# Kernel tuning notes

Measured on AMD Instinct MI355X. Metric: run time of the kernel, lower is better.

## Reference

```python
import jax, jax.numpy as jnp
import numpy as np

WD, WH, WW = 1, 7, 7
N = WD * WH * WW  # 49 tokens per window
LN_EPS = 1e-5


def _make_rel_coords_table():
    rd = np.arange(-(WD - 1), WD, dtype=np.float32)
    rh = np.arange(-(WH - 1), WH, dtype=np.float32)
    rw = np.arange(-(WW - 1), WW, dtype=np.float32)
    g = np.stack(np.meshgrid(rd, rh, rw, indexing='ij'), axis=-1)  # (2wd-1,2wh-1,2ww-1,3)
    eps = 1e-6
    g = g / (np.array([WD, WH, WW], np.float32) - (1.0 - eps))
    g = g * 8.0
    g = np.sign(g) * np.log2(np.abs(g) + 1.0) / np.log2(8.0)
    return g[None].astype(np.float32)  # (1,2wd-1,2wh-1,2ww-1,3)


def _make_rel_pos_index():
    coords = np.stack(np.meshgrid(np.arange(WD), np.arange(WH), np.arange(WW), indexing='ij'))
    cf = coords.reshape(3, -1)  # (3,N)
    rel = cf[:, :, None] - cf[:, None, :]  # (3,N,N)
    rel = rel.transpose(1, 2, 0).astype(np.int64)
    rel[..., 0] += WD - 1
    rel[..., 1] += WH - 1
    rel[..., 2] += WW - 1
    rel[..., 0] *= (2 * WH - 1) * (2 * WW - 1)
    rel[..., 1] *= 2 * WW - 1
    return rel.sum(-1).astype(np.int32)  # (N,N)


def setup_inputs() -> dict:
    key = jax.random.key(0)
    ks = jax.random.split(key, 8)
    B, D, H, W, C = 4, 8, 56, 56, 256
    nh, hid = 8, 4 * C

    def init_w(k, shape, fan_in):
        return (jax.random.normal(k, shape, jnp.float32) / np.sqrt(fan_in)).astype(jnp.float32)

    inp = {
        'x': jax.random.normal(ks[0], (B, D, H, W, C), jnp.float32),
        'qkv_w': init_w(ks[1], (3 * C, C), C),
        'q_bias': jnp.zeros((C,), jnp.float32),
        'v_bias': jnp.zeros((C,), jnp.float32),
        'logit_scale': jnp.full((nh, 1, 1), np.log(10.0), jnp.float32),
        'cpb_w1': init_w(ks[2], (512, 3), 3),
        'cpb_b1': jnp.zeros((512,), jnp.float32),
        'cpb_w2': init_w(ks[3], (nh, 512), 512),
        'proj_w': init_w(ks[4], (C, C), C),
        'proj_b': jnp.zeros((C,), jnp.float32),
        'norm1_g': jnp.ones((C,), jnp.float32),
        'norm1_b': jnp.zeros((C,), jnp.float32),
        'fc1_w': init_w(ks[5], (hid, C), C),
        'fc1_b': jnp.zeros((hid,), jnp.float32),
        'fc2_w': init_w(ks[6], (C, hid), hid),
        'fc2_b': jnp.zeros((C,), jnp.float32),
        'norm2_g': jnp.ones((C,), jnp.float32),
        'norm2_b': jnp.zeros((C,), jnp.float32),
        'rel_coords_table': jnp.asarray(_make_rel_coords_table()),
        'rel_pos_index': jnp.asarray(_make_rel_pos_index()),
    }
    return inp


def _layernorm(x, g, b):
    mu = jnp.mean(x, axis=-1, keepdims=True)
    var = jnp.mean(jnp.square(x - mu), axis=-1, keepdims=True)
    return (x - mu) * jax.lax.rsqrt(var + LN_EPS) * g + b


def _l2norm(x):
    # F.normalize(dim=-1): x / max(||x||, 1e-12)
    n = jnp.sqrt(jnp.sum(jnp.square(x), axis=-1, keepdims=True))
    return x / jnp.maximum(n, 1e-12)


def _forward(x, qkv_w, q_bias, v_bias, logit_scale, cpb_w1, cpb_b1, cpb_w2,
             proj_w, proj_b, norm1_g, norm1_b, fc1_w, fc1_b, fc2_w, fc2_b,
             norm2_g, norm2_b, rel_coords_table, rel_pos_index):
    B, D, H, W, C = x.shape
    nh = logit_scale.shape[0]
    hd = C // nh

    # ---- window partition: (B,D,H,W,C) -> (B_, N, C)
    xw = x.reshape(B, D // WD, WD, H // WH, WH, W // WW, WW, C)
    xw = xw.transpose(0, 1, 3, 5, 2, 4, 6, 7).reshape(-1, N, C)
    Bw = xw.shape[0]

    # ---- qkv with (q_bias, 0, v_bias)
    qkv_bias = jnp.concatenate([q_bias, jnp.zeros_like(q_bias), v_bias])
    qkv = xw @ qkv_w.T + qkv_bias  # (Bw,N,3C)
    qkv = qkv.reshape(Bw, N, 3, nh, hd).transpose(2, 0, 3, 1, 4)
    q, k, v = qkv[0], qkv[1], qkv[2]  # (Bw,nh,N,hd)

    # ---- cosine attention with clamped learned logit scale
    attn = jnp.einsum('bhnd,bhmd->bhnm', _l2norm(q), _l2norm(k))
    scale = jnp.exp(jnp.minimum(logit_scale, jnp.float32(np.log(100.0))))  # (nh,1,1)
    attn = attn * scale

    # ---- CPB-MLP relative position bias
    t = rel_coords_table.reshape(-1, 3)
    hcpb = jax.nn.relu(t @ cpb_w1.T + cpb_b1)
    table = hcpb @ cpb_w2.T  # (T, nh)
    rpb = table[rel_pos_index.reshape(-1)].reshape(N, N, nh).transpose(2, 0, 1)
    rpb = 16.0 * jax.nn.sigmoid(rpb)
    attn = attn + rpb[None]

    attn = jax.nn.softmax(attn, axis=-1)
    out = jnp.einsum('bhnm,bhmd->bhnd', attn, v)
    out = out.transpose(0, 2, 1, 3).reshape(Bw, N, C)
    out = out @ proj_w.T + proj_b

    # ---- window reverse
    xr = out.reshape(B, D // WD, H // WH, W // WW, WD, WH, WW, C)
    xr = xr.transpose(0, 1, 4, 2, 5, 3, 6, 7).reshape(B, D, H, W, C)

    # ---- Swin-v2 post-norm residuals
    x = x + _layernorm(xr, norm1_g, norm1_b)
    h = jax.nn.gelu(x @ fc1_w.T + fc1_b, approximate=False)
    y = h @ fc2_w.T + fc2_b
    x = x + _layernorm(y, norm2_g, norm2_b)
    return x


def reference(x, qkv_w, q_bias, v_bias, logit_scale, cpb_w1, cpb_b1, cpb_w2,
              proj_w, proj_b, norm1_g, norm1_b, fc1_w, fc1_b, fc2_w, fc2_b,
              norm2_g, norm2_b, rel_coords_table, rel_pos_index):
    return _forward(x, qkv_w, q_bias, v_bias, logit_scale, cpb_w1, cpb_b1, cpb_w2,
                    proj_w, proj_b, norm1_g, norm1_b, fc1_w, fc1_b, fc2_w, fc2_b,
                    norm2_g, norm2_b, rel_coords_table, rel_pos_index)
```

## Files before the change

### kernel.cpp

```cpp
#include <hip/hip_runtime.h>
#include <hip/hip_bf16.h>

typedef __attribute__((ext_vector_type(8))) short short8_t;
typedef __attribute__((ext_vector_type(4))) float f32x4;

__device__ __forceinline__ float bf2f(unsigned short u) {
    return __uint_as_float(((unsigned)u) << 16);
}
__device__ __forceinline__ unsigned short f2bf(float f) {
    __hip_bfloat16 h = __float2bfloat16(f);
    return *reinterpret_cast<unsigned short*>(&h);
}

__device__ __forceinline__ float fast_gelu(float v) {
    float ax = fabsf(v) * 0.70710678118f;
    float t  = __builtin_amdgcn_rcpf(1.f + 0.3275911f * ax);
    float poly = t * (0.254829592f + t * (-0.284496736f + t * (1.421413741f
               + t * (-1.453152027f + t * 1.061405429f))));
    float e  = __expf(-ax * ax);
    float er = 1.f - poly * e;
    float s  = (v >= 0.f) ? er : -er;
    return 0.5f * v * (1.f + s);
}

__device__ __forceinline__ void async16(const unsigned short* g, unsigned short* l) {
    __builtin_amdgcn_global_load_lds(
        (const __attribute__((address_space(1))) unsigned int*)g,
        (__attribute__((address_space(3))) unsigned int*)l,
        16, 0, 0);
}

__device__ __forceinline__ int win_row_to_token(int r) {
    int wb = r / 49, n = r - wb * 49;
    int wq = wb & 7, hb = (wb >> 3) & 7, d = (wb >> 6) & 7, b = wb >> 9;
    int hh = n / 7, ww2 = n - hh * 7;
    return ((b * 8 + d) * 56 + hb * 7 + hh) * 56 + wq * 7 + ww2;
}

__global__ __launch_bounds__(256) void conv_kernel(
    const float* __restrict__ src, unsigned short* __restrict__ dst, int n4)
{
    int stride = gridDim.x * 256;
    for (int i = blockIdx.x * 256 + threadIdx.x; i < n4; i += stride) {
        float4 v = *reinterpret_cast<const float4*>(&src[(size_t)i * 4]);
        short4 o;
        o.x = (short)f2bf(v.x); o.y = (short)f2bf(v.y);
        o.z = (short)f2bf(v.z); o.w = (short)f2bf(v.w);
        *reinterpret_cast<short4*>(&dst[(size_t)i * 4]) = o;
    }
}

__global__ __launch_bounds__(256) void conv4_kernel(
    const float* __restrict__ s0, unsigned short* __restrict__ d0, int n0,
    const float* __restrict__ s1, unsigned short* __restrict__ d1, int n1,
    const float* __restrict__ s2, unsigned short* __restrict__ d2, int n2,
    const float* __restrict__ s3, unsigned short* __restrict__ d3, int n3)
{
    int stride = gridDim.x * 256;
    int total = n0 + n1 + n2 + n3;
    for (int i = blockIdx.x * 256 + threadIdx.x; i < total; i += stride) {
        const float* s; unsigned short* d; int j = i;
        if (j < n0) { s = s0; d = d0; }
        else if ((j -= n0) < n1) { s = s1; d = d1; }
        else if ((j -= n1) < n2) { s = s2; d = d2; }
        else { j -= n2; s = s3; d = d3; }
        float4 v = *reinterpret_cast<const float4*>(&s[(size_t)j * 4]);
        short4 o;
        o.x = (short)f2bf(v.x); o.y = (short)f2bf(v.y);
        o.z = (short)f2bf(v.z); o.w = (short)f2bf(v.w);
        *reinterpret_cast<short4*>(&d[(size_t)j * 4]) = o;
    }
}

__global__ __launch_bounds__(256) void prep_table_kernel(
    const float* __restrict__ w1, const float* __restrict__ b1,
    const float* __restrict__ w2, const float* __restrict__ tabin,
    float* __restrict__ tableg)
{
    const int i = blockIdx.x;
    const int t = threadIdx.x;
    const float c0 = tabin[i * 3], c1 = tabin[i * 3 + 1], c2 = tabin[i * 3 + 2];
    float part[8] = {0.f, 0.f, 0.f, 0.f, 0.f, 0.f, 0.f, 0.f};
    for (int j = t; j < 512; j += 256) {
        float hv = fmaxf(c0 * w1[j * 3] + c1 * w1[j * 3 + 1] + c2 * w1[j * 3 + 2] + b1[j], 0.f);
        #pragma unroll
        for (int h = 0; h < 8; ++h) part[h] += hv * w2[h * 512 + j];
    }
    #pragma unroll
    for (int h = 0; h < 8; ++h) {
        float v = part[h];
        v += __shfl_xor(v, 1);  v += __shfl_xor(v, 2);  v += __shfl_xor(v, 4);
        v += __shfl_xor(v, 8);  v += __shfl_xor(v, 16); v += __shfl_xor(v, 32);
        part[h] = v;
    }
    __shared__ float red[4][8];
    const int wv = t >> 6, lane = t & 63;
    if (lane == 0) {
        #pragma unroll
        for (int h = 0; h < 8; ++h) red[wv][h] = part[h];
    }
    __syncthreads();
    if (t < 8) tableg[i * 8 + t] = red[0][t] + red[1][t] + red[2][t] + red[3][t];
}

__global__ __launch_bounds__(256) void prep_expand_kernel(
    const float* __restrict__ logit_scale,
    const float* __restrict__ qb, const float* __restrict__ vb,
    const int* __restrict__ rpi, const float* __restrict__ tableg,
    float* __restrict__ scales, float* __restrict__ rpbf,
    float* __restrict__ qkvb)
{
    const int stride = gridDim.x * 256;
    const int gt = blockIdx.x * 256 + threadIdx.x;
    if (gt < 8) scales[gt] = expf(fminf(logit_scale[gt], 4.6051702f));
    for (int i = gt; i < 768; i += stride) {
        float o;
        if (i < 256) o = qb[i];
        else if (i < 512) o = 0.f;
        else o = vb[i - 512];
        qkvb[i] = o;
    }
    for (int e = gt; e < 32768; e += stride) {
        int h = e >> 12, rem = e & 4095;
        int mi = rem >> 10, ji = (rem >> 8) & 3;
        int r16 = (rem >> 4) & 15, g4 = (rem >> 2) & 3, r = rem & 3;
        int i = mi * 16 + g4 * 4 + r, j = ji * 16 + r16;
        float val = 0.f;
        if (i < 49 && j < 49) {
            float xv = tableg[rpi[i * 49 + j] * 8 + h];
            val = 16.f / (1.f + expf(-xv));
        }
        rpbf[e] = val;
    }
}

template<int ACT, int SCATTER>
__global__ __launch_bounds__(256) void gemm_kernel(
    const unsigned short* __restrict__ A, const unsigned short* __restrict__ W,
    const float* __restrict__ bias, unsigned short* __restrict__ C,
    int M, int N, int K, int ntn)
{
    __shared__ unsigned short smem[16384];
    const int tid = threadIdx.x;
    const int lane = tid & 63, wv = tid >> 6;
    const int wr = wv >> 1, wc = wv & 1;
    const int nwg = gridDim.x;
    const int virt = (blockIdx.x & 7) * (nwg >> 3) + (blockIdx.x >> 3);
    const int bn = virt % ntn, bm = virt / ntn;
    const size_t arow0 = (size_t)bm * 128;
    const size_t brow0 = (size_t)bn * 128;
    const int r16 = lane & 15, g4 = lane >> 4;
    const int srow_l = lane >> 2;
    const int sgran  = (lane & 3) ^ ((srow_l >> 1) & 3);
    f32x4 acc[4][4] = {};

    auto STAGE = [&](int buf, int kt) {
        unsigned short* As = smem + buf * 4096;
        unsigned short* Bs = smem + 8192 + buf * 4096;
        #pragma unroll
        for (int i = 0; i < 2; ++i) {
            int row0 = wv * 32 + i * 16;
            async16(&A[(arow0 + row0 + srow_l) * (size_t)K + kt + sgran * 8], &As[row0 * 32]);
            async16(&W[(brow0 + row0 + srow_l) * (size_t)K + kt + sgran * 8], &Bs[row0 * 32]);
        }
    };
    auto COMPUTE = [&](int buf) {
        unsigned short* As = smem + buf * 4096;
        unsigned short* Bs = smem + 8192 + buf * 4096;
        short8_t af[4], bfr[4];
        const int gsw = g4 ^ ((r16 >> 1) & 3);
        #pragma unroll
        for (int m = 0; m < 4; ++m) {
            int row = wr * 64 + m * 16 + r16;
            af[m] = *reinterpret_cast<const short8_t*>(&As[row * 32 + gsw * 8]);
        }
        #pragma unroll
        for (int n = 0; n < 4; ++n) {
            int row = wc * 64 + n * 16 + r16;
            bfr[n] = *reinterpret_cast<const short8_t*>(&Bs[row * 32 + gsw * 8]);
        }
        #pragma unroll
        for (int m = 0; m < 4; ++m)
            #pragma unroll
            for (int n = 0; n < 4; ++n)
                acc[m][n] = __builtin_amdgcn_mfma_f32_16x16x32_bf16(af[m], bfr[n], acc[m][n], 0, 0, 0);
    };

    const int nk = K >> 5;
    STAGE(0, 0);
    STAGE(1, 32);
    int cur = 0;
    for (int ks = 0; ks < nk - 1; ++ks) {
        asm volatile("s_waitcnt vmcnt(4)" ::: "memory");
        __builtin_amdgcn_sched_barrier(0);
        asm volatile("s_barrier" ::: "memory");
        COMPUTE(cur);
        __builtin_amdgcn_sched_barrier(0);
        asm volatile("s_barrier" ::: "memory");
        if (ks + 2 < nk) STAGE(cur, (ks + 2) << 5);
        cur ^= 1;
    }
    asm volatile("s_waitcnt vmcnt(0)" ::: "memory");
    __builtin_amdgcn_sched_barrier(0);
    asm volatile("s_barrier" ::: "memory");
    COMPUTE(cur);
    __builtin_amdgcn_sched_barrier(0);
    asm volatile("s_barrier" ::: "memory");

    unsigned short* Cs = smem + wv * 2432;
    const int rbase = g4 * 4;
    const int srow = lane >> 3, scol = (lane & 7) * 8;
    const int gcol0 = bn * 128 + wc * 64;
    #pragma unroll
    for (int p = 0; p < 2; ++p) {
        #pragma unroll
        for (int n = 0; n < 4; ++n) {
            float bv = bias[bn * 128 + wc * 64 + n * 16 + r16];
            #pragma unroll
            for (int m2 = 0; m2 < 2; ++m2) {
                int m = p * 2 + m2;
                #pragma unroll
                for (int r = 0; r < 4; ++r) {
                    float v = acc[m][n][r] + bv;
                    if (ACT == 1) v = fast_gelu(v);
                    Cs[(m2 * 16 + rbase + r) * 76 + n * 16 + r16] = f2bf(v);
                }
            }
        }
        #pragma unroll
        for (int rr = 0; rr < 4; ++rr) {
            int lr = rr * 8 + srow;
            int grow = bm * 128 + wr * 64 + p * 32 + lr;
            size_t orow = SCATTER ? (size_t)win_row_to_token(grow) : (size_t)grow;
            short8_t vv = *reinterpret_cast<const short8_t*>(&Cs[lr * 76 + scol]);
            *reinterpret_cast<short8_t*>(&C[orow * (size_t)N + gcol0 + scol]) = vv;
        }
    }
}

__global__ __launch_bounds__(64) void attn_kernel(
    const unsigned short* __restrict__ qkv, const float* __restrict__ scales,
    const float* __restrict__ rpbf, unsigned short* __restrict__ out)
{
    constexpr int QO = 0;
    constexpr int KO = 2560;
    constexpr int VO = 5120;
    constexpr int PO = 0;
    __shared__ unsigned short lds[7424];

    const int blk = blockIdx.x;
    const int h = blk & 7, wb = blk >> 3;
    const int lane = threadIdx.x;
    const int r16 = lane & 15, g4 = lane >> 4;

    const int wq = wb & 7, hb = (wb >> 3) & 7, dd = (wb >> 6) & 7, bb2 = wb >> 9;
    const int tok_base = ((bb2 * 8 + dd) * 56 + hb * 7) * 56 + wq * 7;
    const float sc = scales[h];

    {
        short8_t z = {};
        int d = lane >> 1, j0 = 48 + (lane & 1) * 8;
        *reinterpret_cast<short8_t*>(&lds[VO + d * 72 + j0]) = z;
    }
    #pragma unroll
    for (int sel = 0; sel < 2; ++sel) {
        for (int c = lane; c < 196; c += 64) {
            int row = c >> 2, gi = c & 3;
            int tok = tok_base + (row / 7) * 56 + (row % 7);
            const unsigned short* gp = qkv + (size_t)tok * 768 + sel * 256 + h * 32 + gi * 8;
            short8_t raw = *reinterpret_cast<const short8_t*>(gp);
            float f[8]; float ss = 0.f;
            #pragma unroll
            for (int e = 0; e < 8; ++e) { f[e] = bf2f((unsigned short)raw[e]); ss += f[e] * f[e]; }
            ss += __shfl_xor(ss, 1); ss += __shfl_xor(ss, 2);
            float inv = 1.f / fmaxf(sqrtf(ss), 1e-12f);
            if (sel == 0) inv *= sc;
            short8_t o;
            #pragma unroll
            for (int e = 0; e < 8; ++e) o[e] = (short)f2bf(f[e] * inv);
            *reinterpret_cast<short8_t*>(&lds[(sel ? KO : QO) + row * 40 + gi * 8]) = o;
        }
    }
    for (int c = lane; c < 196; c += 64) {
        int j = c >> 2, gi = c & 3;
        int tok = tok_base + (j / 7) * 56 + (j % 7);
        short8_t raw = *reinterpret_cast<const short8_t*>(
            qkv + (size_t)tok * 768 + 512 + h * 32 + gi * 8);
        #pragma unroll
        for (int e = 0; e < 8; ++e)
            lds[VO + (gi * 8 + e) * 72 + j] = (unsigned short)raw[e];
    }
    __syncthreads();

    short8_t qf[4], kf[4];
    #pragma unroll
    for (int mi = 0; mi < 4; ++mi)
        qf[mi] = *reinterpret_cast<const short8_t*>(&lds[QO + (mi * 16 + r16) * 40 + g4 * 8]);
    #pragma unroll
    for (int ji = 0; ji < 4; ++ji)
        kf[ji] = *reinterpret_cast<const short8_t*>(&lds[KO + (ji * 16 + r16) * 40 + g4 * 8]);
    f32x4 acc[4][4] = {};
    #pragma unroll
    for (int mi = 0; mi < 4; ++mi)
        #pragma unroll
        for (int ji = 0; ji < 4; ++ji)
            acc[mi][ji] = __builtin_amdgcn_mfma_f32_16x16x32_bf16(qf[mi], kf[ji], acc[mi][ji], 0, 0, 0);
    __syncthreads();

    const float* rbf = rpbf + h * 4096 + r16 * 16 + g4 * 4;
    f32x4 rbv[4][4];
    #pragma unroll
    for (int mi = 0; mi < 4; ++mi)
        #pragma unroll
        for (int ji = 0; ji < 4; ++ji)
            rbv[mi][ji] = *reinterpret_cast<const f32x4*>(&rbf[(mi * 4 + ji) * 256]);

    #pragma unroll
    for (int mi = 0; mi < 4; ++mi) {
        #pragma unroll
        for (int r = 0; r < 4; ++r) {
            int i = mi * 16 + g4 * 4 + r;
            float s[4]; float m = -1e30f;
            #pragma unroll
            for (int ji = 0; ji < 4; ++ji) {
                int j = ji * 16 + r16;
                float v = acc[mi][ji][r] + rbv[mi][ji][r];
                s[ji] = (j < 49) ? v : -1e30f;
                m = fmaxf(m, s[ji]);
            }
            m = fmaxf(m, __shfl_xor(m, 1)); m = fmaxf(m, __shfl_xor(m, 2));
            m = fmaxf(m, __shfl_xor(m, 4)); m = fmaxf(m, __shfl_xor(m, 8));
            float p[4]; float sum = 0.f;
            #pragma unroll
            for (int ji = 0; ji < 4; ++ji) {
                p[ji] = (s[ji] > -1e29f) ? __expf(s[ji] - m) : 0.f;
                sum += p[ji];
            }
            sum += __shfl_xor(sum, 1); sum += __shfl_xor(sum, 2);
            sum += __shfl_xor(sum, 4); sum += __shfl_xor(sum, 8);
            float rinv = 1.f / sum;
            #pragma unroll
            for (int ji = 0; ji < 4; ++ji) {
                int j = ji * 16 + r16;
                lds[PO + i * 72 + j] = f2bf(p[ji] * rinv);
            }
        }
    }
    __syncthreads();

    f32x4 acc2[4][2] = {};
    #pragma unroll
    for (int ks = 0; ks < 2; ++ks) {
        short8_t pf[4], vf[2];
        int ko = ks * 32 + g4 * 8;
        #pragma unroll
        for (int mi = 0; mi < 4; ++mi)
            pf[mi] = *reinterpret_cast<const short8_t*>(&lds[PO + (mi * 16 + r16) * 72 + ko]);
        #pragma unroll
        for (int ni = 0; ni < 2; ++ni)
            vf[ni] = *reinterpret_cast<const short8_t*>(&lds[VO + (ni * 16 + r16) * 72 + ko]);
        #pragma unroll
        for (int mi = 0; mi < 4; ++mi)
            #pragma unroll
            for (int ni = 0; ni < 2; ++ni)
                acc2[mi][ni] = __builtin_amdgcn_mfma_f32_16x16x32_bf16(pf[mi], vf[ni], acc2[mi][ni], 0, 0, 0);
    }

    #pragma unroll
    for (int mi = 0; mi < 4; ++mi)
        #pragma unroll
        for (int r = 0; r < 4; ++r) {
            int i = mi * 16 + g4 * 4 + r;
            if (i < 49) {
                size_t ob = (size_t)(wb * 49 + i) * 256 + h * 32;
                out[ob + r16]      = f2bf(acc2[mi][0][r]);
                out[ob + 16 + r16] = f2bf(acc2[mi][1][r]);
            }
        }
}

template<int BASE_F32, int OUT_F32>
__global__ __launch_bounds__(256) void ln_add_kernel(
    const void* __restrict__ basev, const unsigned short* __restrict__ vin,
    const float* __restrict__ gg, const float* __restrict__ bb,
    void* __restrict__ outv)
{
    int token = blockIdx.x * 4 + (threadIdx.x >> 6);
    int lane = threadIdx.x & 63;
    size_t off = (size_t)token * 256 + lane * 4;
    short4 raw = *reinterpret_cast<const short4*>(&vin[off]);
    float f0 = bf2f((unsigned short)raw.x), f1 = bf2f((unsigned short)raw.y);
    float f2 = bf2f((unsigned short)raw.z), f3 = bf2f((unsigned short)raw.w);
    float s  = f0 + f1 + f2 + f3;
    float s2 = f0 * f0 + f1 * f1 + f2 * f2 + f3 * f3;
    #pragma unroll
    for (int m = 32; m >= 1; m >>= 1) { s += __shfl_xor(s, m, 64); s2 += __shfl_xor(s2, m, 64); }
    float mu = s * 0.00390625f;
    float var = s2 * 0.00390625f - mu * mu;
    float inv = rsqrtf(var + 1e-5f);

    float b0, b1v, b2, b3;
    if (BASE_F32) {
        float4 braw = *reinterpret_cast<const float4*>(&((const float*)basev)[off]);
        b0 = braw.x; b1v = braw.y; b2 = braw.z; b3 = braw.w;
    } else {
        short4 braw = *reinterpret_cast<const short4*>(&((const unsigned short*)basev)[off]);
        b0 = bf2f((unsigned short)braw.x); b1v = bf2f((unsigned short)braw.y);
        b2 = bf2f((unsigned short)braw.z); b3 = bf2f((unsigned short)braw.w);
    }
    float4 graw = *reinterpret_cast<const float4*>(&gg[lane * 4]);
    float4 brw2 = *reinterpret_cast<const float4*>(&bb[lane * 4]);
    float o0 = b0 + (f0 - mu) * inv * graw.x + brw2.x;
    float o1 = b1v + (f1 - mu) * inv * graw.y + brw2.y;
    float o2 = b2 + (f2 - mu) * inv * graw.z + brw2.z;
    float o3 = b3 + (f3 - mu) * inv * graw.w + brw2.w;
    if (OUT_F32) {
        float4 o; o.x = o0; o.y = o1; o.z = o2; o.w = o3;
        *reinterpret_cast<float4*>(&((float*)outv)[off]) = o;
    } else {
        short4 o;
        o.x = (short)f2bf(o0); o.y = (short)f2bf(o1);
        o.z = (short)f2bf(o2); o.w = (short)f2bf(o3);
        *reinterpret_cast<short4*>(&((unsigned short*)outv)[off]) = o;
    }
}

extern "C" void kernel_launch(void* const* d_in, const int* in_sizes, int n_in,
                              void* d_out, int out_size, void* d_ws, size_t ws_size,
                              hipStream_t stream) {
    const float* x      = (const float*)d_in[0];
    const float* qkv_w  = (const float*)d_in[1];
    const float* q_bias = (const float*)d_in[2];
    const float* v_bias = (const float*)d_in[3];
    const float* lscale = (const float*)d_in[4];
    const float* cpb_w1 = (const float*)d_in[5];
    const float* cpb_b1 = (const float*)d_in[6];
    const float* cpb_w2 = (const float*)d_in[7];
    const float* proj_w = (const float*)d_in[8];
    const float* proj_b = (const float*)d_in[9];
    const float* n1g    = (const float*)d_in[10];
    const float* n1b    = (const float*)d_in[11];
    const float* fc1_w  = (const float*)d_in[12];
    const float* fc1_b  = (const float*)d_in[13];
    const float* fc2_w  = (const float*)d_in[14];
    const float* fc2_b  = (const float*)d_in[15];
    const float* n2g    = (const float*)d_in[16];
    const float* n2b    = (const float*)d_in[17];
    const float* rct    = (const float*)d_in[18];
    const int*   rpi    = (const int*)d_in[19];

    char* ws = (char*)d_ws;
    unsigned short* qkv    = (unsigned short*)(ws);
    unsigned short* hbuf   = (unsigned short*)(ws);
    unsigned short* attn_o = (unsigned short*)(ws + 154140672);
    unsigned short* xb     = (unsigned short*)(ws + 205520896);
    unsigned short* x1     = (unsigned short*)(ws + 205520896);
    unsigned short* projy  = (unsigned short*)(ws + 256901120);
    unsigned short* wqkv   = (unsigned short*)(ws + 308281344);
    unsigned short* wproj  = (unsigned short*)(ws + 308674560);
    unsigned short* wfc1   = (unsigned short*)(ws + 308805632);
    unsigned short* wfc2   = (unsigned short*)(ws + 309329920);
    float*          rpbf   = (float*)(ws + 309854208);
    float*          scales = (float*)(ws + 310378496);
    float*          qkvb   = (float*)(ws + 310378528);
    float*          tableg = (float*)(ws + 310381600);

    const int M = 100352;

    conv_kernel<<<2048, 256, 0, stream>>>(x, xb, 25690112 / 4);
    conv4_kernel<<<768, 256, 0, stream>>>(qkv_w, wqkv, 49152,
                                          proj_w, wproj, 16384,
                                          fc1_w, wfc1, 65536,
                                          fc2_w, wfc2, 65536);
    prep_table_kernel<<<169, 256, 0, stream>>>(cpb_w1, cpb_b1, cpb_w2, rct, tableg);
    prep_expand_kernel<<<128, 256, 0, stream>>>(lscale, q_bias, v_bias, rpi, tableg,
                                                scales, rpbf, qkvb);
    gemm_kernel<0, 0><<<4704, 256, 0, stream>>>(xb, wqkv, qkvb, qkv, M, 768, 256, 6);
    attn_kernel<<<16384, 64, 0, stream>>>(qkv, scales, rpbf, attn_o);
    gemm_kernel<0, 1><<<1568, 256, 0, stream>>>(attn_o, wproj, proj_b, projy, M, 256, 256, 2);
    ln_add_kernel<0, 0><<<25088, 256, 0, stream>>>(xb, projy, n1g, n1b, x1);
    gemm_kernel<1, 0><<<6272, 256, 0, stream>>>(x1, wfc1, fc1_b, hbuf, M, 1024, 256, 8);
    gemm_kernel<0, 0><<<1568, 256, 0, stream>>>(hbuf, wfc2, fc2_b, projy, M, 256, 1024, 2);
    ln_add_kernel<0, 1><<<25088, 256, 0, stream>>>(x1, projy, n2g, n2b, d_out);
}
```

Before: 487.2 us.

## Fuse layernorm and residual add into proj and fc2 GEMM epilogues

Adds a 512-thread GEMM kernel with 128x256 tiles, so each block holds full rows of the 256-wide output. Row mean and variance are reduced in LDS, and the layernorm plus residual add is applied in the epilogue. This replaces the separate proj/fc2 GEMMs and ln_add kernels, removing the round trip of the intermediate projy buffer and two launches. The cost is larger tiles with fewer blocks (784), more LDS and registers per block, and possibly lower occupancy for the K=1024 fc2 GEMM.

```diff
diff --git a/kernel.cpp b/kernel.cpp
--- a/kernel.cpp
+++ b/kernel.cpp
@@ -238,6 +238,171 @@
     }
 }
 
+template<int SCATTER, int OUT_F32>
+__global__ __launch_bounds__(512) void gemm_ln_kernel(
+    const unsigned short* __restrict__ A, const unsigned short* __restrict__ W,
+    const float* __restrict__ bias, const unsigned short* __restrict__ resid,
+    const float* __restrict__ gamma, const float* __restrict__ beta,
+    void* __restrict__ Cv, int M, int K)
+{
+    __shared__ unsigned short smem[24576];
+    const int tid = threadIdx.x;
+    const int lane = tid & 63, wv = tid >> 6;
+    const int wr = wv >> 2, wc = wv & 3;
+    const int nwg = gridDim.x;
+    const int bm = (blockIdx.x & 7) * (nwg >> 3) + (blockIdx.x >> 3);
+    const size_t arow0 = (size_t)bm * 128;
+    const int r16 = lane & 15, g4 = lane >> 4;
+    const int srow_l = lane >> 2;
+    const int sgran = (lane & 3) ^ ((srow_l >> 1) & 3);
+    f32x4 acc[4][4] = {};
+
+    auto STAGE = [&](int buf, int kt) {
+        unsigned short* As = smem + buf * 4096;
+        unsigned short* Bs = smem + 8192 + buf * 8192;
+        async16(&A[(arow0 + wv * 16 + srow_l) * (size_t)K + kt + sgran * 8],
+                &As[(wv * 16) * 32]);
+        #pragma unroll
+        for (int i = 0; i < 2; ++i) {
+            int row0 = wv * 32 + i * 16;
+            async16(&W[(size_t)(row0 + srow_l) * K + kt + sgran * 8], &Bs[row0 * 32]);
+        }
+    };
+    auto COMPUTE = [&](int buf) {
+        unsigned short* As = smem + buf * 4096;
+        unsigned short* Bs = smem + 8192 + buf * 8192;
+        short8_t af[4], bfr[4];
+        const int gsw = g4 ^ ((r16 >> 1) & 3);
+        #pragma unroll
+        for (int m = 0; m < 4; ++m) {
+            int row = wr * 64 + m * 16 + r16;
+            af[m] = *reinterpret_cast<const short8_t*>(&As[row * 32 + gsw * 8]);
+        }
+        #pragma unroll
+        for (int n = 0; n < 4; ++n) {
+            int row = wc * 64 + n * 16 + r16;
+            bfr[n] = *reinterpret_cast<const short8_t*>(&Bs[row * 32 + gsw * 8]);
+        }
+        #pragma unroll
+        for (int m = 0; m < 4; ++m)
+            #pragma unroll
+            for (int n = 0; n < 4; ++n)
+                acc[m][n] = __builtin_amdgcn_mfma_f32_16x16x32_bf16(af[m], bfr[n], acc[m][n], 0, 0, 0);
+    };
+
+    const int nk = K >> 5;
+    STAGE(0, 0);
+    STAGE(1, 32);
+    int cur = 0;
+    for (int ks = 0; ks < nk - 1; ++ks) {
+        asm volatile("s_waitcnt vmcnt(3)" ::: "memory");
+        __builtin_amdgcn_sched_barrier(0);
+        asm volatile("s_barrier" ::: "memory");
+        COMPUTE(cur);
+        __builtin_amdgcn_sched_barrier(0);
+        asm volatile("s_barrier" ::: "memory");
+        if (ks + 2 < nk) STAGE(cur, (ks + 2) << 5);
+        cur ^= 1;
+    }
+    asm volatile("s_waitcnt vmcnt(0)" ::: "memory");
+    __builtin_amdgcn_sched_barrier(0);
+    asm volatile("s_barrier" ::: "memory");
+    COMPUTE(cur);
+    __builtin_amdgcn_sched_barrier(0);
+    asm volatile("s_barrier" ::: "memory");
+
+    float bv[4];
+    #pragma unroll
+    for (int n = 0; n < 4; ++n) bv[n] = bias[wc * 64 + n * 16 + r16];
+    float* psum  = reinterpret_cast<float*>(smem + 19456);
+    float* psq   = psum + 512;
+    float* stats = psq + 512;
+    #pragma unroll
+    for (int m = 0; m < 4; ++m) {
+        #pragma unroll
+        for (int r = 0; r < 4; ++r) {
+            float s = 0.f, s2 = 0.f;
+            #pragma unroll
+            for (int n = 0; n < 4; ++n) {
+                float v = acc[m][n][r] + bv[n];
+                s += v; s2 += v * v;
+            }
+            s  += __shfl_xor(s, 1);  s  += __shfl_xor(s, 2);
+            s  += __shfl_xor(s, 4);  s  += __shfl_xor(s, 8);
+            s2 += __shfl_xor(s2, 1); s2 += __shfl_xor(s2, 2);
+            s2 += __shfl_xor(s2, 4); s2 += __shfl_xor(s2, 8);
+            if (r16 == 0) {
+                int row = wr * 64 + m * 16 + g4 * 4 + r;
+                psum[row * 4 + wc] = s;
+                psq[row * 4 + wc]  = s2;
+            }
+        }
+    }
+    __syncthreads();
+    if (tid < 128) {
+        f32x4 a = *reinterpret_cast<const f32x4*>(&psum[tid * 4]);
+        f32x4 b = *reinterpret_cast<const f32x4*>(&psq[tid * 4]);
+        float mu  = (a[0] + a[1] + a[2] + a[3]) * 0.00390625f;
+        float ex2 = (b[0] + b[1] + b[2] + b[3]) * 0.00390625f;
+        stats[tid * 2]     = mu;
+        stats[tid * 2 + 1] = rsqrtf(ex2 - mu * mu + 1e-5f);
+    }
+    __syncthreads();
+
+    unsigned short* Cs = smem + wv * 2432;
+    const int rbase = g4 * 4;
+    const int srow = lane >> 3, scol = (lane & 7) * 8;
+    const int gcol0 = wc * 64;
+    f32x4 gm0 = *reinterpret_cast<const f32x4*>(&gamma[gcol0 + scol]);
+    f32x4 gm1 = *reinterpret_cast<const f32x4*>(&gamma[gcol0 + scol + 4]);
+    f32x4 bt0 = *reinterpret_cast<const f32x4*>(&beta[gcol0 + scol]);
+    f32x4 bt1 = *reinterpret_cast<const f32x4*>(&beta[gcol0 + scol + 4]);
+    #pragma unroll
+    for (int p = 0; p < 2; ++p) {
+        #pragma unroll
+        for (int n = 0; n < 4; ++n)
+            #pragma unroll
+            for (int m2 = 0; m2 < 2; ++m2)
+                #pragma unroll
+                for (int r = 0; r < 4; ++r)
+                    Cs[(m2 * 16 + rbase + r) * 76 + n * 16 + r16] =
+                        f2bf(acc[p * 2 + m2][n][r] + bv[n]);
+        #pragma unroll
+        for (int rr = 0; rr < 4; ++rr) {
+            int lr = rr * 8 + srow;
+            int lrow = wr * 64 + p * 32 + lr;
+            int grow = bm * 128 + lrow;
+            size_t orow = SCATTER ? (size_t)win_row_to_token(grow) : (size_t)grow;
+            float mu  = stats[lrow * 2];
+            float inv = stats[lrow * 2 + 1];
+            short8_t cv = *reinterpret_cast<const short8_t*>(&Cs[lr * 76 + scol]);
+            short8_t rv = *reinterpret_cast<const short8_t*>(&resid[orow * 256 + gcol0 + scol]);
+            float o[8];
+            #pragma unroll
+            for (int e = 0; e < 8; ++e) {
+                float g = (e < 4) ? gm0[e] : gm1[e - 4];
+                float bb = (e < 4) ? bt0[e] : bt1[e - 4];
+                o[e] = bf2f((unsigned short)rv[e])
+                     + (bf2f((unsigned short)cv[e]) - mu) * inv * g + bb;
+            }
+            if (OUT_F32) {
+                float* outp = (float*)Cv + orow * 256 + gcol0 + scol;
+                f32x4 o0, o1;
+                #pragma unroll
+                for (int e = 0; e < 4; ++e) { o0[e] = o[e]; o1[e] = o[e + 4]; }
+                *reinterpret_cast<f32x4*>(outp)     = o0;
+                *reinterpret_cast<f32x4*>(outp + 4) = o1;
+            } else {
+                unsigned short* outp = (unsigned short*)Cv + orow * 256 + gcol0 + scol;
+                short8_t ov;
+                #pragma unroll
+                for (int e = 0; e < 8; ++e) ov[e] = (short)f2bf(o[e]);
+                *reinterpret_cast<short8_t*>(outp) = ov;
+            }
+        }
+    }
+}
+
 __global__ __launch_bounds__(64) void attn_kernel(
     const unsigned short* __restrict__ qkv, const float* __restrict__ scales,
     const float* __restrict__ rpbf, unsigned short* __restrict__ out)
@@ -377,52 +542,6 @@
                 out[ob + 16 + r16] = f2bf(acc2[mi][1][r]);
             }
         }
-}
-
-template<int BASE_F32, int OUT_F32>
-__global__ __launch_bounds__(256) void ln_add_kernel(
-    const void* __restrict__ basev, const unsigned short* __restrict__ vin,
-    const float* __restrict__ gg, const float* __restrict__ bb,
-    void* __restrict__ outv)
-{
-    int token = blockIdx.x * 4 + (threadIdx.x >> 6);
-    int lane = threadIdx.x & 63;
-    size_t off = (size_t)token * 256 + lane * 4;
-    short4 raw = *reinterpret_cast<const short4*>(&vin[off]);
-    float f0 = bf2f((unsigned short)raw.x), f1 = bf2f((unsigned short)raw.y);
-    float f2 = bf2f((unsigned short)raw.z), f3 = bf2f((unsigned short)raw.w);
-    float s  = f0 + f1 + f2 + f3;
-    float s2 = f0 * f0 + f1 * f1 + f2 * f2 + f3 * f3;
-    #pragma unroll
-    for (int m = 32; m >= 1; m >>= 1) { s += __shfl_xor(s, m, 64); s2 += __shfl_xor(s2, m, 64); }
-    float mu = s * 0.00390625f;
-    float var = s2 * 0.00390625f - mu * mu;
-    float inv = rsqrtf(var + 1e-5f);
-
-    float b0, b1v, b2, b3;
-    if (BASE_F32) {
-        float4 braw = *reinterpret_cast<const float4*>(&((const float*)basev)[off]);
-        b0 = braw.x; b1v = braw.y; b2 = braw.z; b3 = braw.w;
-    } else {
-        short4 braw = *reinterpret_cast<const short4*>(&((const unsigned short*)basev)[off]);
-        b0 = bf2f((unsigned short)braw.x); b1v = bf2f((unsigned short)braw.y);
-        b2 = bf2f((unsigned short)braw.z); b3 = bf2f((unsigned short)braw.w);
-    }
-    float4 graw = *reinterpret_cast<const float4*>(&gg[lane * 4]);
-    float4 brw2 = *reinterpret_cast<const float4*>(&bb[lane * 4]);
-    float o0 = b0 + (f0 - mu) * inv * graw.x + brw2.x;
-    float o1 = b1v + (f1 - mu) * inv * graw.y + brw2.y;
-    float o2 = b2 + (f2 - mu) * inv * graw.z + brw2.z;
-    float o3 = b3 + (f3 - mu) * inv * graw.w + brw2.w;
-    if (OUT_F32) {
-        float4 o; o.x = o0; o.y = o1; o.z = o2; o.w = o3;
-        *reinterpret_cast<float4*>(&((float*)outv)[off]) = o;
-    } else {
-        short4 o;
-        o.x = (short)f2bf(o0); o.y = (short)f2bf(o1);
-        o.z = (short)f2bf(o2); o.w = (short)f2bf(o3);
-        *reinterpret_cast<short4*>(&((unsigned short*)outv)[off]) = o;
-    }
 }
 
 extern "C" void kernel_launch(void* const* d_in, const int* in_sizes, int n_in,
@@ -455,7 +574,6 @@
     unsigned short* attn_o = (unsigned short*)(ws + 154140672);
     unsigned short* xb     = (unsigned short*)(ws + 205520896);
     unsigned short* x1     = (unsigned short*)(ws + 205520896);
-    unsigned short* projy  = (unsigned short*)(ws + 256901120);
     unsigned short* wqkv   = (unsigned short*)(ws + 308281344);
     unsigned short* wproj  = (unsigned short*)(ws + 308674560);
     unsigned short* wfc1   = (unsigned short*)(ws + 308805632);
@@ -477,9 +595,9 @@
                                                 scales, rpbf, qkvb);
     gemm_kernel<0, 0><<<4704, 256, 0, stream>>>(xb, wqkv, qkvb, qkv, M, 768, 256, 6);
     attn_kernel<<<16384, 64, 0, stream>>>(qkv, scales, rpbf, attn_o);
-    gemm_kernel<0, 1><<<1568, 256, 0, stream>>>(attn_o, wproj, proj_b, projy, M, 256, 256, 2);
-    ln_add_kernel<0, 0><<<25088, 256, 0, stream>>>(xb, projy, n1g, n1b, x1);
+    gemm_ln_kernel<1, 0><<<784, 512, 0, stream>>>(attn_o, wproj, proj_b, xb, n1g, n1b,
+                                                  x1, M, 256);
     gemm_kernel<1, 0><<<6272, 256, 0, stream>>>(x1, wfc1, fc1_b, hbuf, M, 1024, 256, 8);
-    gemm_kernel<0, 0><<<1568, 256, 0, stream>>>(hbuf, wfc2, fc2_b, projy, M, 256, 1024, 2);
-    ln_add_kernel<0, 1><<<25088, 256, 0, stream>>>(x1, projy, n2g, n2b, d_out);
-}
+    gemm_ln_kernel<0, 1><<<784, 512, 0, stream>>>(hbuf, wfc2, fc2_b, x1, n2g, n2b,
+                                                  d_out, M, 1024);
+}
```

New measurement: 465.9 us. -4.4%, faster.
